# Kernel tuning notes

Hardware: AMD Instinct MI355X
Metric: run time of the kernel (lower is better)

Reference implementation:

```python
import jax, jax.numpy as jnp
import numpy as np

B, S, D, H, N, E = 4, 2048, 512, 8, 1024, 16384


def setup_inputs() -> dict:
    key = jax.random.key(0)
    ks = jax.random.split(key, 16)
    rn = lambda k, shp, s=0.02: jax.random.normal(k, shp, jnp.float32) * s
    x = jax.random.normal(ks[0], (B, S, D), jnp.float32)
    edge_index = jax.random.randint(ks[1], (2, E), 0, N)
    # unique sorted node positions per batch (equivalent to node_mask with N ones)
    node_indices = jnp.sort(
        jax.vmap(lambda k: jax.random.permutation(k, S)[:N])(jax.random.split(ks[2], B)),
        axis=1,
    )
    z = lambda shp: jnp.zeros(shp, jnp.float32)
    o = lambda shp: jnp.ones(shp, jnp.float32)
    return {
        "x": x,
        "edge_index": edge_index,
        "node_indices": node_indices,
        "Wq": rn(ks[3], (D, D)), "bq": z((D,)),
        "Wk": rn(ks[4], (D, D)), "bk": z((D,)),
        "Wv": rn(ks[5], (D, D)), "bv": z((D,)),
        "Wo": rn(ks[6], (D, D)), "bo": z((D,)),
        "Wf1": rn(ks[7], (D, 4 * D)), "bf1": z((4 * D,)),
        "Wf2": rn(ks[8], (4 * D, D)), "bf2": z((D,)),
        "g1": o((D,)), "be1": z((D,)),
        "g2": o((D,)), "be2": z((D,)),
        "g3": o((D,)), "be3": z((D,)),
        "Wg": rn(ks[9], (2 * D, D)), "bg": z((D,)),
        "Wgs": rn(ks[10], (D, D)), "Wgn": rn(ks[11], (D, D)), "bgn": z((D,)),
    }


def _ln(t, g, b, eps=1e-5):
    m = t.mean(-1, keepdims=True)
    v = ((t - m) ** 2).mean(-1, keepdims=True)
    return (t - m) * jax.lax.rsqrt(v + eps) * g + b


def reference(x, edge_index, node_indices, Wq, bq, Wk, bk, Wv, bv, Wo, bo,
              Wf1, bf1, Wf2, bf2, g1, be1, g2, be2, g3, be3, Wg, bg,
              Wgs, Wgn, bgn):
    Bs, Ss, Ds = x.shape
    Hn = H
    hd = Ds // Hn
    Nn = node_indices.shape[1]

    # --- self-attention (pre-norm, residual; dropout = eval identity) ---
    nx = _ln(x, g1, be1)
    q = (nx @ Wq + bq).reshape(Bs, Ss, Hn, hd).transpose(0, 2, 1, 3)
    k = (nx @ Wk + bk).reshape(Bs, Ss, Hn, hd).transpose(0, 2, 1, 3)
    v = (nx @ Wv + bv).reshape(Bs, Ss, Hn, hd).transpose(0, 2, 1, 3)
    scores = jnp.einsum('bhqd,bhkd->bhqk', q, k) / jnp.sqrt(jnp.float32(hd))
    attn = jax.nn.softmax(scores, axis=-1)
    ao = jnp.einsum('bhqk,bhkd->bhqd', attn, v).transpose(0, 2, 1, 3).reshape(Bs, Ss, Ds)
    x = x + ao @ Wo + bo

    # --- gather -> GNN -> scatter with sigmoid gate fusion ---
    nx2 = _ln(x, g2, be2)
    bidx = jnp.arange(Bs)[:, None]
    nodes = nx2[bidx, node_indices]                       # [B, N, D] gather
    src, dst = edge_index[0], edge_index[1]
    msgs = nodes[:, src, :]                               # [B, E, D]
    agg = jax.vmap(lambda m: jax.ops.segment_sum(m, dst, num_segments=Nn))(msgs)
    upd = jax.nn.relu(nodes @ Wgs + agg @ Wgn + bgn)      # GCN-like update
    gnn_out = jnp.zeros_like(nx2).at[bidx, node_indices].set(upd)  # scatter-back
    gate = jax.nn.sigmoid(jnp.concatenate([nx2, gnn_out], axis=-1) @ Wg + bg)
    x = x + gate * gnn_out + (1.0 - gate) * nx2

    # --- feed-forward ---
    nx3 = _ln(x, g3, be3)
    x = x + jax.nn.gelu(nx3 @ Wf1 + bf1, approximate=False) @ Wf2 + bf2
    return x
```

## Files before the change

kernel.cpp:

```cpp
#include <hip/hip_runtime.h>
#include <math.h>

using u16 = unsigned short;
using u32 = unsigned int;

typedef __attribute__((ext_vector_type(8))) short bf16x8;
typedef __attribute__((ext_vector_type(4))) float f32x4;

#define B_   4
#define S_   2048
#define D_   512
#define H_   8
#define HD_  64
#define N_   1024
#define E_   16384
#define DFF_ 2048
#define BS_  (B_ * S_)
#define BN_  (B_ * N_)
#define QSCALE 0.18033688011112042f
#define KSTRIDE 68
#define KSPLIT 2

__device__ __forceinline__ float bf2f(u16 u) {
  u32 v = (u32)u << 16; float f; __builtin_memcpy(&f, &v, 4); return f;
}
__device__ __forceinline__ u16 f2bf(float f) {
  u32 u; __builtin_memcpy(&u, &f, 4);
  u = u + 0x7fffu + ((u >> 16) & 1u);
  return (u16)(u >> 16);
}
__device__ __forceinline__ float bflo(u32 w) {
  u32 v = w << 16; float f; __builtin_memcpy(&f, &v, 4); return f;
}
__device__ __forceinline__ float bfhi(u32 w) {
  u32 v = w & 0xffff0000u; float f; __builtin_memcpy(&f, &v, 4); return f;
}
__device__ __forceinline__ u32 fbits(float f) { u32 u; __builtin_memcpy(&u, &f, 4); return u; }

__global__ __launch_bounds__(256) void tpose_all(const float* __restrict__ Wq, const float* __restrict__ Wk,
                                                 const float* __restrict__ Wv, const float* __restrict__ Wo,
                                                 const float* __restrict__ Wgs, const float* __restrict__ Wgn,
                                                 const float* __restrict__ Wg, const float* __restrict__ Wf1,
                                                 const float* __restrict__ Wf2, u16* __restrict__ wsbase) {
  __shared__ u16 t[32][33];
  const int z = blockIdx.z;
  const float* src; int C, r0, c0, ds, co; long doff;
  const long SL = 262144;
  switch (z) {
    case 0:  src = Wq;  C = 512;  r0 = 0;   c0 = 0;    ds = 512;  co = 0;   doff = 0;       break;
    case 1:  src = Wk;  C = 512;  r0 = 0;   c0 = 0;    ds = 512;  co = 0;   doff = 1 * SL;  break;
    case 2:  src = Wv;  C = 512;  r0 = 0;   c0 = 0;    ds = 512;  co = 0;   doff = 2 * SL;  break;
    case 3:  src = Wo;  C = 512;  r0 = 0;   c0 = 0;    ds = 512;  co = 0;   doff = 3 * SL;  break;
    case 4:  src = Wg;  C = 512;  r0 = 0;   c0 = 0;    ds = 1024; co = 0;   doff = 4 * SL;  break;
    case 5:  src = Wg;  C = 512;  r0 = 512; c0 = 0;    ds = 1024; co = 512; doff = 4 * SL;  break;
    case 6:  src = Wgs; C = 512;  r0 = 0;   c0 = 0;    ds = 1024; co = 0;   doff = 6 * SL;  break;
    case 7:  src = Wgn; C = 512;  r0 = 0;   c0 = 0;    ds = 1024; co = 512; doff = 6 * SL;  break;
    case 8: case 9: case 10: case 11:
             src = Wf1; C = 2048; r0 = 0;   c0 = (z - 8) * 512;  ds = 512;  co = 0; doff = 8 * SL;  break;
    default: src = Wf2; C = 512;  r0 = (z - 12) * 512; c0 = 0;   ds = 2048; co = (z - 12) * 512; doff = 12 * SL; break;
  }
  u16* dst = wsbase + doff;
  int rb = blockIdx.x * 32, cb = blockIdx.y * 32 + c0;
  int tx = threadIdx.x, ty = threadIdx.y;
  #pragma unroll
  for (int i = ty; i < 32; i += 8) t[i][tx] = f2bf(src[(long)(r0 + rb + i) * C + cb + tx]);
  __syncthreads();
  #pragma unroll
  for (int i = ty; i < 32; i += 8) dst[(long)(cb + i) * ds + co + rb + tx] = t[tx][i];
}

__global__ void packb_k(const float* __restrict__ bq, const float* __restrict__ bk,
                        const float* __restrict__ bv, float* __restrict__ o) {
  int i = blockIdx.x * 256 + threadIdx.x;
  if (i < 512) o[i] = bq[i];
  else if (i < 1024) o[i] = bk[i - 512];
  else if (i < 1536) o[i] = bv[i - 1024];
}

__global__ __launch_bounds__(256) void ln_k(const float* __restrict__ x, const float* __restrict__ g,
                                            const float* __restrict__ be, u16* __restrict__ out) {
  __shared__ float red[8];
  long row = blockIdx.x;
  int t = threadIdx.x;
  const float* xr = x + row * D_;
  float2 v = *(const float2*)(xr + 2 * t);
  float s = v.x + v.y, sq = v.x * v.x + v.y * v.y;
  #pragma unroll
  for (int m = 32; m >= 1; m >>= 1) { s += __shfl_xor(s, m, 64); sq += __shfl_xor(sq, m, 64); }
  if ((t & 63) == 0) { red[t >> 6] = s; red[4 + (t >> 6)] = sq; }
  __syncthreads();
  s = red[0] + red[1] + red[2] + red[3];
  sq = red[4] + red[5] + red[6] + red[7];
  float mean = s * (1.f / D_);
  float var = sq * (1.f / D_) - mean * mean;
  float rs = rsqrtf(fmaxf(var, 0.f) + 1e-5f);
  float2 gw = *(const float2*)(g + 2 * t);
  float2 bw = *(const float2*)(be + 2 * t);
  u32 o = (u32)f2bf((v.x - mean) * rs * gw.x + bw.x) | ((u32)f2bf((v.y - mean) * rs * gw.y + bw.y) << 16);
  *(u32*)&out[row * D_ + 2 * t] = o;
}

__device__ __forceinline__ void async_cp16(const u16* g, u16* l) {
  __builtin_amdgcn_global_load_lds((const __attribute__((address_space(1))) void*)g,
                                   (__attribute__((address_space(3))) void*)l, 16, 0, 0);
}

enum { EPI_QKV3, EPI_XF32, EPI_BF, EPI_RELU_SCATTER, EPI_GELU };

template <int EPI, bool CAT = false, int TM = 128>
__global__ __launch_bounds__(256) void gemm_k(const u16* __restrict__ A, const u16* __restrict__ A2,
                                              const u16* __restrict__ Bt, const float* __restrict__ bias,
                                              const void* src, void* out, const int* __restrict__ rowmap,
                                              int M, int N, int K) {
  constexpr int MT = TM / 32;
  __shared__ __align__(16) u16 As[2][TM * 32];
  __shared__ __align__(16) u16 Bs[2][4096];
  int tid = threadIdx.x;
  int lane = tid & 63;
  int wn = (tid >> 6) & 1;
  int wm = (tid >> 7) & 1;
  int nwg = gridDim.x * gridDim.y;
  int orig = blockIdx.y * gridDim.x + blockIdx.x;
  int wgid = ((orig & 7) * (nwg >> 3)) + (orig >> 3);
  int bx = wgid % gridDim.x;
  int by = wgid / gridDim.x;
  long m0 = (long)by * TM;
  long n0 = (long)bx * 128;

  f32x4 acc[MT][4];
  {
    f32x4 z = {0.f, 0.f, 0.f, 0.f};
    #pragma unroll
    for (int i = 0; i < MT; i++)
      #pragma unroll
      for (int j = 0; j < 4; j++) acc[i][j] = z;
  }

  int srow = tid >> 2;
  int skoff = (tid & 3) * 8;
  const int astride = CAT ? 512 : K;
  const u16* Ag  = A + (m0 + srow) * (long)astride + skoff;
  const u16* A2g = CAT ? (A2 + (m0 + srow) * (long)astride + skoff) : nullptr;
  const u16* Bg  = Bt + (n0 + srow) * (long)K + skoff;
  int rsel = lane & 15;
  int kchunk = (lane >> 4) * 8;

  auto stage = [&](int buf, int kts) {
    const u16* Asrc = (CAT && kts >= 512) ? (A2g + (kts - 512)) : (Ag + kts);
    if constexpr (TM == 32) {
      if (tid < 128) async_cp16(Asrc, &As[buf][tid * 8]);
    } else {
      async_cp16(Asrc, &As[buf][tid * 8]);
      if constexpr (TM == 128) async_cp16(Asrc + (long)64 * astride, &As[buf][2048 + tid * 8]);
    }
    async_cp16(Bg + kts, &Bs[buf][tid * 8]);
    async_cp16(Bg + (long)64 * K + kts, &Bs[buf][2048 + tid * 8]);
  };

  stage(0, 0);
  __syncthreads();
  int buf = 0;
  for (int kt = 0; kt < K; kt += 32) {
    if (kt + 32 < K) stage(buf ^ 1, kt + 32);
    bf16x8 af[MT], bfv[4];
    #pragma unroll
    for (int mt = 0; mt < MT; mt++)
      af[mt] = *(const bf16x8*)&As[buf][(wm * (TM / 2) + mt * 16 + rsel) * 32 + kchunk];
    #pragma unroll
    for (int nt = 0; nt < 4; nt++)
      bfv[nt] = *(const bf16x8*)&Bs[buf][(wn * 64 + nt * 16 + rsel) * 32 + kchunk];
    #pragma unroll
    for (int mt = 0; mt < MT; mt++)
      #pragma unroll
      for (int nt = 0; nt < 4; nt++)
        acc[mt][nt] = __builtin_amdgcn_mfma_f32_16x16x32_bf16(af[mt], bfv[nt], acc[mt][nt], 0, 0, 0);
    __syncthreads();
    buf ^= 1;
  }

  int rbase = (lane >> 4) * 4;
  int cbase = lane & 15;
  #pragma unroll
  for (int mt = 0; mt < MT; mt++) {
    #pragma unroll
    for (int nt = 0; nt < 4; nt++) {
      long col = n0 + wn * 64 + nt * 16 + cbase;
      float bv = bias ? bias[col] : 0.f;
      long row0 = m0 + wm * (TM / 2) + mt * 16 + rbase;
      float vals[4];
      #pragma unroll
      for (int r = 0; r < 4; r++) vals[r] = acc[mt][nt][r] + bv;
      if constexpr (EPI == EPI_QKV3) {
        long which = col >> 9;
        long cc = col & 511;
        long b = row0 >> 11;
        long h = cc >> 6, d = cc & 63;
        if (which == 2) {
          long sI0 = row0 & 2047;
          uint2 w;
          w.x = (u32)f2bf(vals[0]) | ((u32)f2bf(vals[1]) << 16);
          w.y = (u32)f2bf(vals[2]) | ((u32)f2bf(vals[3]) << 16);
          *(uint2*)&((u16*)out)[2 * (long)BS_ * D_ + (((b * H_ + h) * HD_) + d) * S_ + sI0] = w;
        } else {
          #pragma unroll
          for (int r = 0; r < 4; r++) {
            long sI = (row0 + r) & 2047;
            float v2 = (which == 0) ? vals[r] * QSCALE : vals[r];
            ((u16*)out)[which * (long)BS_ * D_ + (((b * H_ + h) * S_) + sI) * HD_ + d] = f2bf(v2);
          }
        }
      } else {
        #pragma unroll
        for (int r = 0; r < 4; r++) {
          long row = row0 + r;
          float val = vals[r];
          if constexpr (EPI == EPI_XF32) {
            ((float*)out)[row * N + col] = val + ((const float*)src)[row * N + col];
          } else if constexpr (EPI == EPI_BF) {
            ((u16*)out)[row * N + col] = f2bf(val);
          } else if constexpr (EPI == EPI_RELU_SCATTER) {
            long orow = rowmap[row];
            ((u16*)out)[orow * D_ + col] = f2bf(fmaxf(val, 0.f));
          } else if constexpr (EPI == EPI_GELU) {
            ((u16*)out)[row * N + col] = f2bf(0.5f * val * (1.f + erff(val * 0.70710678118654752f)));
          }
        }
      }
    }
  }
}

__global__ __launch_bounds__(256) void attn_k(const u16* __restrict__ Q, const u16* __restrict__ Kv,
                                              const u16* __restrict__ VT, u16* __restrict__ Opart,
                                              float* __restrict__ Lp) {
  __shared__ __align__(16) u16 Ks[64 * KSTRIDE];
  __shared__ __align__(16) u16 Vs[64 * KSTRIDE];
  int tid = threadIdx.x;
  int lane = tid & 63;
  int wave = tid >> 6;
  int col = lane & 15;
  int quad = lane >> 4;
  int bh = blockIdx.y;
  int q0 = blockIdx.x * 128;
  int khalf = blockIdx.z;
  long base = (long)bh * S_;
  long vbase = (long)bh * HD_ * S_;

  const u16* qpa = Q + (base + q0 + wave * 32 + col) * HD_;
  const u16* qpb = qpa + 16 * HD_;
  bf16x8 bqa0 = *(const bf16x8*)(qpa + quad * 8);
  bf16x8 bqa1 = *(const bf16x8*)(qpa + 32 + quad * 8);
  bf16x8 bqb0 = *(const bf16x8*)(qpb + quad * 8);
  bf16x8 bqb1 = *(const bf16x8*)(qpb + 32 + quad * 8);

  float la = 0.f, lb = 0.f;
  f32x4 accA[4], accB[4];
  {
    f32x4 z = {0.f, 0.f, 0.f, 0.f};
    #pragma unroll
    for (int mt = 0; mt < 4; mt++) { accA[mt] = z; accB[mt] = z; }
  }

  int srow = tid >> 2;
  int sdc = (tid & 3) * 16;
  const bool hiQ = (quad >= 2);
  const int s0 = (quad & 1) * 2;
  const int a0 = (s0 * 16 + col + wave * 64) * 4;
  const int a1 = ((s0 + 1) * 16 + col + wave * 64) * 4;

  int kt0 = khalf * (S_ / KSPLIT);
  for (int kt = kt0; kt < kt0 + S_ / KSPLIT; kt += 64) {
    __syncthreads();
    {
      const u16* kg = Kv + (base + kt + srow) * HD_ + sdc;
      *(bf16x8*)&Ks[srow * KSTRIDE + sdc]     = *(const bf16x8*)kg;
      *(bf16x8*)&Ks[srow * KSTRIDE + sdc + 8] = *(const bf16x8*)(kg + 8);
      const u16* vg = VT + (vbase + (long)srow * S_) + kt + sdc;
      *(bf16x8*)&Vs[srow * KSTRIDE + sdc]     = *(const bf16x8*)vg;
      *(bf16x8*)&Vs[srow * KSTRIDE + sdc + 8] = *(const bf16x8*)(vg + 8);
    }
    __syncthreads();

    f32x4 sa[4], sb[4];
    __builtin_amdgcn_s_setprio(1);
    #pragma unroll
    for (int nt = 0; nt < 4; nt++) {
      bf16x8 ak0 = *(const bf16x8*)&Ks[(nt * 16 + col) * KSTRIDE + quad * 8];
      bf16x8 ak1 = *(const bf16x8*)&Ks[(nt * 16 + col) * KSTRIDE + 32 + quad * 8];
      f32x4 z = {0.f, 0.f, 0.f, 0.f};
      z = __builtin_amdgcn_mfma_f32_16x16x32_bf16(ak0, bqa0, z, 0, 0, 0);
      z = __builtin_amdgcn_mfma_f32_16x16x32_bf16(ak1, bqa1, z, 0, 0, 0);
      sa[nt] = z;
      f32x4 y = {0.f, 0.f, 0.f, 0.f};
      y = __builtin_amdgcn_mfma_f32_16x16x32_bf16(ak0, bqb0, y, 0, 0, 0);
      y = __builtin_amdgcn_mfma_f32_16x16x32_bf16(ak1, bqb1, y, 0, 0, 0);
      sb[nt] = y;
    }
    __builtin_amdgcn_s_setprio(0);

    u32 pka[4][2], pkb[4][2];
    #pragma unroll
    for (int nt = 0; nt < 4; nt++) {
      #pragma unroll
      for (int r = 0; r < 4; r++) { sa[nt][r] = __builtin_amdgcn_exp2f(sa[nt][r]); sb[nt][r] = __builtin_amdgcn_exp2f(sb[nt][r]); }
      la += (sa[nt][0] + sa[nt][1]) + (sa[nt][2] + sa[nt][3]);
      lb += (sb[nt][0] + sb[nt][1]) + (sb[nt][2] + sb[nt][3]);
      pka[nt][0] = __builtin_amdgcn_perm(fbits(sa[nt][1]), fbits(sa[nt][0]), 0x07060302u);
      pka[nt][1] = __builtin_amdgcn_perm(fbits(sa[nt][3]), fbits(sa[nt][2]), 0x07060302u);
      pkb[nt][0] = __builtin_amdgcn_perm(fbits(sb[nt][1]), fbits(sb[nt][0]), 0x07060302u);
      pkb[nt][1] = __builtin_amdgcn_perm(fbits(sb[nt][3]), fbits(sb[nt][2]), 0x07060302u);
    }

    union { u32 d[4]; bf16x8 v; } ba0, ba1, bb0, bb1;
    {
      u32 sA = hiQ ? pka[1][0] : pka[0][0];
      u32 sB = hiQ ? pka[1][1] : pka[0][1];
      ba0.d[0] = __builtin_amdgcn_ds_bpermute(a0, sA);
      ba0.d[1] = __builtin_amdgcn_ds_bpermute(a0, sB);
      ba0.d[2] = __builtin_amdgcn_ds_bpermute(a1, sA);
      ba0.d[3] = __builtin_amdgcn_ds_bpermute(a1, sB);
      u32 sC = hiQ ? pka[3][0] : pka[2][0];
      u32 sD = hiQ ? pka[3][1] : pka[2][1];
      ba1.d[0] = __builtin_amdgcn_ds_bpermute(a0, sC);
      ba1.d[1] = __builtin_amdgcn_ds_bpermute(a0, sD);
      ba1.d[2] = __builtin_amdgcn_ds_bpermute(a1, sC);
      ba1.d[3] = __builtin_amdgcn_ds_bpermute(a1, sD);
      u32 tA = hiQ ? pkb[1][0] : pkb[0][0];
      u32 tB = hiQ ? pkb[1][1] : pkb[0][1];
      bb0.d[0] = __builtin_amdgcn_ds_bpermute(a0, tA);
      bb0.d[1] = __builtin_amdgcn_ds_bpermute(a0, tB);
      bb0.d[2] = __builtin_amdgcn_ds_bpermute(a1, tA);
      bb0.d[3] = __builtin_amdgcn_ds_bpermute(a1, tB);
      u32 tC = hiQ ? pkb[3][0] : pkb[2][0];
      u32 tD = hiQ ? pkb[3][1] : pkb[2][1];
      bb1.d[0] = __builtin_amdgcn_ds_bpermute(a0, tC);
      bb1.d[1] = __builtin_amdgcn_ds_bpermute(a0, tD);
      bb1.d[2] = __builtin_amdgcn_ds_bpermute(a1, tC);
      bb1.d[3] = __builtin_amdgcn_ds_bpermute(a1, tD);
    }

    __builtin_amdgcn_s_setprio(1);
    #pragma unroll
    for (int mt = 0; mt < 4; mt++) {
      bf16x8 av0 = *(const bf16x8*)&Vs[(mt * 16 + col) * KSTRIDE + quad * 8];
      bf16x8 av1 = *(const bf16x8*)&Vs[(mt * 16 + col) * KSTRIDE + 32 + quad * 8];
      accA[mt] = __builtin_amdgcn_mfma_f32_16x16x32_bf16(av0, ba0.v, accA[mt], 0, 0, 0);
      accA[mt] = __builtin_amdgcn_mfma_f32_16x16x32_bf16(av1, ba1.v, accA[mt], 0, 0, 0);
      accB[mt] = __builtin_amdgcn_mfma_f32_16x16x32_bf16(av0, bb0.v, accB[mt], 0, 0, 0);
      accB[mt] = __builtin_amdgcn_mfma_f32_16x16x32_bf16(av1, bb1.v, accB[mt], 0, 0, 0);
    }
    __builtin_amdgcn_s_setprio(0);
  }

  la += __shfl_xor(la, 16, 64);
  la += __shfl_xor(la, 32, 64);
  lb += __shfl_xor(lb, 16, 64);
  lb += __shfl_xor(lb, 32, 64);

  int b = bh >> 3, h = bh & 7;
  long qrowA = (long)(b * S_) + q0 + wave * 32 + col;
  u16* Pp = Opart + (long)khalf * BS_ * D_;
  if (quad == 0) {
    float* lr = Lp + ((long)(khalf * 32 + bh)) * S_ + q0 + wave * 32;
    lr[col] = la;
    lr[16 + col] = lb;
  }
  u16* opA = Pp + qrowA * D_ + h * HD_ + quad * 4;
  u16* opB = Pp + (qrowA + 16) * D_ + h * HD_ + quad * 4;
  #pragma unroll
  for (int mt = 0; mt < 4; mt++) {
    uint2 w;
    w.x = (u32)f2bf(accA[mt][0]) | ((u32)f2bf(accA[mt][1]) << 16);
    w.y = (u32)f2bf(accA[mt][2]) | ((u32)f2bf(accA[mt][3]) << 16);
    *(uint2*)(opA + mt * 16) = w;
    uint2 v;
    v.x = (u32)f2bf(accB[mt][0]) | ((u32)f2bf(accB[mt][1]) << 16);
    v.y = (u32)f2bf(accB[mt][2]) | ((u32)f2bf(accB[mt][3]) << 16);
    *(uint2*)(opB + mt * 16) = v;
  }
}

__global__ __launch_bounds__(256) void acomb_k(const u16* __restrict__ P, const float* __restrict__ Lp,
                                               u16* __restrict__ AO) {
  long i = (long)blockIdx.x * 256 + threadIdx.x;
  long e0 = i * 4;
  long tok = e0 >> 9;
  int hh = (int)((e0 >> 6) & 7);
  long s = tok & 2047;
  long bb = tok >> 11;
  long bh = bb * 8 + hh;
  float l = 0.f;
  float v0 = 0.f, v1 = 0.f, v2 = 0.f, v3 = 0.f;
  #pragma unroll
  for (int k = 0; k < KSPLIT; k++) {
    uint2 a = ((const uint2*)(P + (long)k * BS_ * D_))[i];
    v0 += bflo(a.x); v1 += bfhi(a.x);
    v2 += bflo(a.y); v3 += bfhi(a.y);
    l += Lp[((long)(k * 32) + bh) * S_ + s];
  }
  float inv = 1.f / l;
  uint2 o;
  o.x = (u32)f2bf(v0 * inv) | ((u32)f2bf(v1 * inv) << 16);
  o.y = (u32)f2bf(v2 * inv) | ((u32)f2bf(v3 * inv) << 16);
  ((uint2*)AO)[i] = o;
}

__global__ __launch_bounds__(128) void gather_k(const u16* __restrict__ nx2, const int* __restrict__ nidx,
                                                int* __restrict__ rowmap, u16* __restrict__ Acat) {
  int bn = blockIdx.x;
  int t = threadIdx.x;
  long srow = (long)(bn >> 10) * S_ + nidx[bn];
  if (t == 0) rowmap[bn] = (int)srow;
  const u32* sp = (const u32*)(nx2 + srow * D_);
  u32* dp = (u32*)(Acat + (long)bn * 1024);
  dp[t] = sp[t];
  dp[t + 128] = sp[t + 128];
}

#define DEG_CAP 256
__global__ __launch_bounds__(256) void agg_k(const int* __restrict__ ei, u16* __restrict__ Acat) {
  __shared__ int cnt;
  __shared__ int lst[DEG_CAP];
  int n = blockIdx.x;
  int t = threadIdx.x;
  if (t == 0) cnt = 0;
  __syncthreads();
  const int* dst = ei + E_;
  for (int e = t; e < E_; e += 256) {
    if (dst[e] == n) {
      int idx = atomicAdd(&cnt, 1);
      if (idx < DEG_CAP) lst[idx] = ei[e];
    }
  }
  __syncthreads();
  int mcnt = cnt < DEG_CAP ? cnt : DEG_CAP;
  float2 acc[4] = {{0.f, 0.f}, {0.f, 0.f}, {0.f, 0.f}, {0.f, 0.f}};
  for (int i = 0; i < mcnt; i++) {
    long s = lst[i];
    #pragma unroll
    for (int b = 0; b < 4; b++) {
      u32 w = *(const u32*)&Acat[((long)(b * N_) + s) * 1024 + 2 * t];
      acc[b].x += bflo(w);
      acc[b].y += bfhi(w);
    }
  }
  #pragma unroll
  for (int b = 0; b < 4; b++) {
    u32 r = (u32)f2bf(acc[b].x) | ((u32)f2bf(acc[b].y) << 16);
    *(u32*)&Acat[((long)(b * N_) + n) * 1024 + 512 + 2 * t] = r;
  }
}

__global__ __launch_bounds__(256) void combln_k(const float* __restrict__ x1, const u16* __restrict__ gpre,
                                                const u16* __restrict__ gnn, const u16* __restrict__ nx2,
                                                const float* __restrict__ g3, const float* __restrict__ be3,
                                                float* __restrict__ x2, u16* __restrict__ nx3) {
  __shared__ float red[8];
  long row = blockIdx.x;
  int t = threadIdx.x;
  long off = row * D_ + 2 * t;
  float2 a = *(const float2*)(x1 + off);
  u32 gp = *(const u32*)(gpre + off);
  u32 gn = *(const u32*)(gnn + off);
  u32 nv = *(const u32*)(nx2 + off);
  float g0 = 1.f / (1.f + __expf(-bflo(gp)));
  float g1 = 1.f / (1.f + __expf(-bfhi(gp)));
  float t0 = a.x + g0 * bflo(gn) + (1.f - g0) * bflo(nv);
  float t1 = a.y + g1 * bfhi(gn) + (1.f - g1) * bfhi(nv);
  float2 w = {t0, t1};
  *(float2*)(x2 + off) = w;
  float s = t0 + t1, sq = t0 * t0 + t1 * t1;
  #pragma unroll
  for (int m = 32; m >= 1; m >>= 1) { s += __shfl_xor(s, m, 64); sq += __shfl_xor(sq, m, 64); }
  if ((t & 63) == 0) { red[t >> 6] = s; red[4 + (t >> 6)] = sq; }
  __syncthreads();
  s = red[0] + red[1] + red[2] + red[3];
  sq = red[4] + red[5] + red[6] + red[7];
  float mean = s * (1.f / D_);
  float var = sq * (1.f / D_) - mean * mean;
  float rs = rsqrtf(fmaxf(var, 0.f) + 1e-5f);
  float2 gw = *(const float2*)(g3 + 2 * t);
  float2 bw = *(const float2*)(be3 + 2 * t);
  u32 o = (u32)f2bf((t0 - mean) * rs * gw.x + bw.x) | ((u32)f2bf((t1 - mean) * rs * gw.y + bw.y) << 16);
  *(u32*)&nx3[off] = o;
}

extern "C" void kernel_launch(void* const* d_in, const int* in_sizes, int n_in,
                              void* d_out, int out_size, void* d_ws, size_t ws_size,
                              hipStream_t stream) {
  const float* x  = (const float*)d_in[0];
  const int* ei   = (const int*)d_in[1];
  const int* nidx = (const int*)d_in[2];
  const float* Wq = (const float*)d_in[3];   const float* bq = (const float*)d_in[4];
  const float* Wk = (const float*)d_in[5];   const float* bk = (const float*)d_in[6];
  const float* Wv = (const float*)d_in[7];   const float* bv = (const float*)d_in[8];
  const float* Wo = (const float*)d_in[9];   const float* bo = (const float*)d_in[10];
  const float* Wf1 = (const float*)d_in[11]; const float* bf1 = (const float*)d_in[12];
  const float* Wf2 = (const float*)d_in[13]; const float* bf2v = (const float*)d_in[14];
  const float* g1 = (const float*)d_in[15];  const float* be1 = (const float*)d_in[16];
  const float* g2 = (const float*)d_in[17];  const float* be2 = (const float*)d_in[18];
  const float* g3 = (const float*)d_in[19];  const float* be3 = (const float*)d_in[20];
  const float* Wg = (const float*)d_in[21];  const float* bg = (const float*)d_in[22];
  const float* Wgs = (const float*)d_in[23]; const float* Wgn = (const float*)d_in[24];
  const float* bgn = (const float*)d_in[25];

  const size_t MB8 = (size_t)8 * 1024 * 1024;
  char* base = (char*)d_ws;
  const size_t SLOT = (size_t)512 * 512 * 2;
  u16* WqT     = (u16*)(base + 0 * SLOT);
  u16* WoT     = (u16*)(base + 3 * SLOT);
  u16* WgFullT = (u16*)(base + 4 * SLOT);
  u16* WgsgnT  = (u16*)(base + 6 * SLOT);
  u16* Wf1T    = (u16*)(base + 8 * SLOT);
  u16* Wf2T    = (u16*)(base + 12 * SLOT);

  char* RA   = base + 16 * SLOT;
  char* Rqb  = RA + MB8;
  char* Rkb  = Rqb + MB8;
  char* Rvb  = Rkb + MB8;
  char* Rac  = Rvb + MB8;
  char* Rag  = Rac + MB8;
  char* Rx2  = Rag + MB8;
  char* RM   = Rx2 + 2 * MB8;

  u16* nx   = (u16*)RA;   u16* ao  = (u16*)RA;   u16* gnn = (u16*)RA;  u16* nx3 = (u16*)RA;
  u16* qb   = (u16*)Rqb;
  float* x1 = (float*)Rqb;
  u16* nx2  = (u16*)Rvb;
  u16* Opart = (u16*)Rac;
  u16* Acat = (u16*)Rac;
  u16* gpre = (u16*)Rac;
  float* x2 = (float*)Rx2;
  u16* ffh  = (u16*)Rqb;
  int* rowmap = (int*)RM;
  float* qkvb = (float*)(RM + 16384);
  float* Lpart = (float*)(RM + 32768);

  dim3 tb(32, 8);
  tpose_all<<<dim3(16, 16, 16), tb, 0, stream>>>(Wq, Wk, Wv, Wo, Wgs, Wgn, Wg, Wf1, Wf2, (u16*)base);
  packb_k<<<6, 256, 0, stream>>>(bq, bk, bv, qkvb);

  ln_k<<<BS_, 256, 0, stream>>>(x, g1, be1, nx);
  gemm_k<EPI_QKV3, false, 128><<<dim3(12, 64), 256, 0, stream>>>(nx, nullptr, WqT, qkvb, nullptr, qb, nullptr, BS_, 1536, 512);
  attn_k<<<dim3(S_ / 128, B_ * H_, KSPLIT), 256, 0, stream>>>(qb, qb + (long)BS_ * D_, qb + 2 * (long)BS_ * D_, Opart, Lpart);
  acomb_k<<<(BS_ * D_) / (256 * 4), 256, 0, stream>>>(Opart, Lpart, ao);
  gemm_k<EPI_XF32, false, 32><<<dim3(4, 256), 256, 0, stream>>>(ao, nullptr, WoT, bo, x, x1, nullptr, BS_, 512, 512);

  ln_k<<<BS_, 256, 0, stream>>>(x1, g2, be2, nx2);
  gather_k<<<BN_, 128, 0, stream>>>(nx2, nidx, rowmap, Acat);
  hipMemsetAsync(gnn, 0, (size_t)BS_ * D_ * 2, stream);
  agg_k<<<N_, 256, 0, stream>>>(ei, Acat);
  gemm_k<EPI_RELU_SCATTER, false, 32><<<dim3(4, 128), 256, 0, stream>>>(Acat, nullptr, WgsgnT, bgn, nullptr, gnn, rowmap, BN_, 512, 1024);

  gemm_k<EPI_BF, true, 32><<<dim3(4, 256), 256, 0, stream>>>(nx2, gnn, WgFullT, bg, nullptr, gpre, nullptr, BS_, 512, 1024);
  combln_k<<<BS_, 256, 0, stream>>>(x1, gpre, gnn, nx2, g3, be3, x2, nx3);

  gemm_k<EPI_GELU, false, 128><<<dim3(16, 64), 256, 0, stream>>>(nx3, nullptr, Wf1T, bf1, nullptr, ffh, nullptr, BS_, DFF_, 512);
  gemm_k<EPI_XF32, false, 32><<<dim3(4, 256), 256, 0, stream>>>(ffh, nullptr, Wf2T, bf2v, x2, (float*)d_out, nullptr, BS_, 512, DFF_);
}
```

Before: 417.5 us.

## Triple-buffer GEMM LDS staging with vmcnt waits and XOR-swizzled k-chunks

The GEMM main loop moves from a two-buffer pipeline with two __syncthreads per step to three LDS buffers. It prefetches two stages ahead and uses explicit s_waitcnt vmcnt plus a single s_barrier per iteration. The k-chunk offsets for both the global-to-LDS copies and the LDS fragment reads are XOR-swizzled by row to reduce LDS bank conflicts. The s_setprio hints are removed from the attention kernel. The third buffer raises LDS use per block, which may reduce occupancy, and the hand-counted vmcnt values must match the number of outstanding async copies per stage.

```diff
diff --git a/kernel.cpp b/kernel.cpp
--- a/kernel.cpp
+++ b/kernel.cpp
@@ -113,8 +113,8 @@
                                               const void* src, void* out, const int* __restrict__ rowmap,
                                               int M, int N, int K) {
   constexpr int MT = TM / 32;
-  __shared__ __align__(16) u16 As[2][TM * 32];
-  __shared__ __align__(16) u16 Bs[2][4096];
+  __shared__ __align__(16) u16 As[3][TM * 32];
+  __shared__ __align__(16) u16 Bs[3][4096];
   int tid = threadIdx.x;
   int lane = tid & 63;
   int wn = (tid >> 6) & 1;
@@ -136,46 +136,56 @@
       for (int j = 0; j < 4; j++) acc[i][j] = z;
   }
 
-  int srow = tid >> 2;
-  int skoff = (tid & 3) * 8;
   const int astride = CAT ? 512 : K;
-  const u16* Ag  = A + (m0 + srow) * (long)astride + skoff;
-  const u16* A2g = CAT ? (A2 + (m0 + srow) * (long)astride + skoff) : nullptr;
-  const u16* Bg  = Bt + (n0 + srow) * (long)K + skoff;
+  int ta = (TM == 32) ? (tid & 127) : tid;
+  int srowA = ta >> 2;
+  int skA = (((ta & 3) ^ ((ta >> 3) & 3)) * 8);
+  int srowB = tid >> 2;
+  int skB = (((tid & 3) ^ ((tid >> 3) & 3)) * 8);
+  const u16* AgA  = A + (m0 + srowA) * (long)astride + skA;
+  const u16* A2gA = CAT ? (A2 + (m0 + srowA) * (long)astride + skA) : nullptr;
+  const u16* BgB  = Bt + (n0 + srowB) * (long)K + skB;
   int rsel = lane & 15;
-  int kchunk = (lane >> 4) * 8;
+  int kchunk = (((lane >> 4) ^ ((rsel >> 1) & 3)) * 8);
 
   auto stage = [&](int buf, int kts) {
-    const u16* Asrc = (CAT && kts >= 512) ? (A2g + (kts - 512)) : (Ag + kts);
+    const u16* Asrc = (CAT && kts >= 512) ? (A2gA + (kts - 512)) : (AgA + kts);
     if constexpr (TM == 32) {
-      if (tid < 128) async_cp16(Asrc, &As[buf][tid * 8]);
+      async_cp16(Asrc, &As[buf][ta * 8]);
     } else {
       async_cp16(Asrc, &As[buf][tid * 8]);
-      if constexpr (TM == 128) async_cp16(Asrc + (long)64 * astride, &As[buf][2048 + tid * 8]);
-    }
-    async_cp16(Bg + kts, &Bs[buf][tid * 8]);
-    async_cp16(Bg + (long)64 * K + kts, &Bs[buf][2048 + tid * 8]);
+      async_cp16(Asrc + (long)64 * astride, &As[buf][2048 + tid * 8]);
+    }
+    async_cp16(BgB + kts, &Bs[buf][tid * 8]);
+    async_cp16(BgB + (long)64 * K + kts, &Bs[buf][2048 + tid * 8]);
   };
 
+  const int T = K / 32;
   stage(0, 0);
-  __syncthreads();
-  int buf = 0;
-  for (int kt = 0; kt < K; kt += 32) {
-    if (kt + 32 < K) stage(buf ^ 1, kt + 32);
+  stage(1, 32);
+  int b = 0;
+  for (int t = 0; t < T; ++t) {
+    if (t == T - 1) {
+      asm volatile("s_waitcnt vmcnt(0)" ::: "memory");
+    } else {
+      if constexpr (TM == 128) asm volatile("s_waitcnt vmcnt(4)" ::: "memory");
+      else                     asm volatile("s_waitcnt vmcnt(3)" ::: "memory");
+    }
+    __builtin_amdgcn_s_barrier();
     bf16x8 af[MT], bfv[4];
     #pragma unroll
     for (int mt = 0; mt < MT; mt++)
-      af[mt] = *(const bf16x8*)&As[buf][(wm * (TM / 2) + mt * 16 + rsel) * 32 + kchunk];
+      af[mt] = *(const bf16x8*)&As[b][(wm * (TM / 2) + mt * 16 + rsel) * 32 + kchunk];
     #pragma unroll
     for (int nt = 0; nt < 4; nt++)
-      bfv[nt] = *(const bf16x8*)&Bs[buf][(wn * 64 + nt * 16 + rsel) * 32 + kchunk];
+      bfv[nt] = *(const bf16x8*)&Bs[b][(wn * 64 + nt * 16 + rsel) * 32 + kchunk];
     #pragma unroll
     for (int mt = 0; mt < MT; mt++)
       #pragma unroll
       for (int nt = 0; nt < 4; nt++)
         acc[mt][nt] = __builtin_amdgcn_mfma_f32_16x16x32_bf16(af[mt], bfv[nt], acc[mt][nt], 0, 0, 0);
-    __syncthreads();
-    buf ^= 1;
+    if (t + 2 < T) stage((t + 2) % 3, (t + 2) * 32);
+    if (++b == 3) b = 0;
   }
 
   int rbase = (lane >> 4) * 4;
@@ -193,20 +203,20 @@
       if constexpr (EPI == EPI_QKV3) {
         long which = col >> 9;
         long cc = col & 511;
-        long b = row0 >> 11;
+        long b2 = row0 >> 11;
         long h = cc >> 6, d = cc & 63;
         if (which == 2) {
           long sI0 = row0 & 2047;
           uint2 w;
           w.x = (u32)f2bf(vals[0]) | ((u32)f2bf(vals[1]) << 16);
           w.y = (u32)f2bf(vals[2]) | ((u32)f2bf(vals[3]) << 16);
-          *(uint2*)&((u16*)out)[2 * (long)BS_ * D_ + (((b * H_ + h) * HD_) + d) * S_ + sI0] = w;
+          *(uint2*)&((u16*)out)[2 * (long)BS_ * D_ + (((b2 * H_ + h) * HD_) + d) * S_ + sI0] = w;
         } else {
           #pragma unroll
           for (int r = 0; r < 4; r++) {
             long sI = (row0 + r) & 2047;
             float v2 = (which == 0) ? vals[r] * QSCALE : vals[r];
-            ((u16*)out)[which * (long)BS_ * D_ + (((b * H_ + h) * S_) + sI) * HD_ + d] = f2bf(v2);
+            ((u16*)out)[which * (long)BS_ * D_ + (((b2 * H_ + h) * S_) + sI) * HD_ + d] = f2bf(v2);
           }
         }
       } else {
@@ -282,7 +292,6 @@
     __syncthreads();
 
     f32x4 sa[4], sb[4];
-    __builtin_amdgcn_s_setprio(1);
     #pragma unroll
     for (int nt = 0; nt < 4; nt++) {
       bf16x8 ak0 = *(const bf16x8*)&Ks[(nt * 16 + col) * KSTRIDE + quad * 8];
@@ -296,7 +305,6 @@
       y = __builtin_amdgcn_mfma_f32_16x16x32_bf16(ak1, bqb1, y, 0, 0, 0);
       sb[nt] = y;
     }
-    __builtin_amdgcn_s_setprio(0);
 
     u32 pka[4][2], pkb[4][2];
     #pragma unroll
@@ -339,7 +347,6 @@
       bb1.d[3] = __builtin_amdgcn_ds_bpermute(a1, tD);
     }
 
-    __builtin_amdgcn_s_setprio(1);
     #pragma unroll
     for (int mt = 0; mt < 4; mt++) {
       bf16x8 av0 = *(const bf16x8*)&Vs[(mt * 16 + col) * KSTRIDE + quad * 8];
@@ -349,7 +356,6 @@
       accB[mt] = __builtin_amdgcn_mfma_f32_16x16x32_bf16(av0, bb0.v, accB[mt], 0, 0, 0);
       accB[mt] = __builtin_amdgcn_mfma_f32_16x16x32_bf16(av1, bb1.v, accB[mt], 0, 0, 0);
     }
-    __builtin_amdgcn_s_setprio(0);
   }
 
   la += __shfl_xor(la, 16, 64);
```

Result: faster. 407.5 us (-2.4%).
